# Optimization experiments

Hardware: AMD Instinct MI355X
Metric: run time of the kernel (lower is better)

Reference implementation:

```python
import jax, jax.numpy as jnp
import numpy as np

D_MODEL = 2048
HEADS = 16
HEAD_DIM = D_MODEL // HEADS
INNER = 8192
SEQ = 2048
EPS = 1e-5


def _layernorm(x, g, b):
    mu = jnp.mean(x, axis=-1, keepdims=True)
    var = jnp.mean(jnp.square(x - mu), axis=-1, keepdims=True)
    return (x - mu) * jax.lax.rsqrt(var + EPS) * g + b


def setup_inputs() -> dict:
    key = jax.random.key(0)
    ks = jax.random.split(key, 10)
    s = 0.02
    return {
        "x": jax.random.normal(ks[0], (1, SEQ, D_MODEL), dtype=jnp.float32),
        "C_w": jax.random.normal(ks[1], (D_MODEL, 3 * D_MODEL), dtype=jnp.float32) * s,
        "C_b": jnp.zeros((3 * D_MODEL,), dtype=jnp.float32),
        "lin_w": jax.random.normal(ks[2], (D_MODEL, D_MODEL), dtype=jnp.float32) * s,
        "lin_b": jnp.zeros((D_MODEL,), dtype=jnp.float32),
        "ff1_w": jax.random.normal(ks[3], (D_MODEL, INNER), dtype=jnp.float32) * s,
        "ff1_b": jnp.zeros((INNER,), dtype=jnp.float32),
        "ff2_w": jax.random.normal(ks[4], (INNER, D_MODEL), dtype=jnp.float32) * s,
        "ff2_b": jnp.zeros((D_MODEL,), dtype=jnp.float32),
        "ln1_g": jnp.ones((D_MODEL,), dtype=jnp.float32),
        "ln1_b": jnp.zeros((D_MODEL,), dtype=jnp.float32),
        "ln2_g": jnp.ones((D_MODEL,), dtype=jnp.float32),
        "ln2_b": jnp.zeros((D_MODEL,), dtype=jnp.float32),
    }


def reference(x, C_w, C_b, lin_w, lin_b, ff1_w, ff1_b, ff2_w, ff2_b,
              ln1_g, ln1_b, ln2_g, ln2_b):
    b, s, d = x.shape
    c = x @ C_w + C_b                       # [b, s, 3d]
    q, k, v = jnp.split(c, 3, axis=2)
    q = q.reshape(b, s, HEADS, HEAD_DIM)
    k = k.reshape(b, s, HEADS, HEAD_DIM)
    v = v.reshape(b, s, HEADS, HEAD_DIM)
    # NOTE: source scales by sqrt(d_model), NOT sqrt(head_dim)
    qk = jnp.einsum('bqhd,bkhd->bhqk', q, k) / jnp.sqrt(jnp.float32(d))
    causal = jnp.tril(jnp.ones((s, s), dtype=bool))  # [s, s]
    qk = jnp.where(causal[None, None, :, :], qk, -jnp.inf)
    scores = jax.nn.softmax(qk, axis=3)
    out = jnp.einsum('bhqk,bkhd->bqhd', scores, v).reshape(b, s, d)
    attn = out @ lin_w + lin_b
    h1 = _layernorm(x + attn, ln1_g, ln1_b)
    ff = jax.nn.gelu(h1 @ ff1_w + ff1_b, approximate=False) @ ff2_w + ff2_b
    return _layernorm(h1 + ff, ln2_g, ln2_b)
```

## Files before the change

### kernel.cpp

```cpp
#include <hip/hip_runtime.h>
#include <hip/hip_bf16.h>

#define SEQ 2048
#define DM 2048
#define NH 16
#define HD 128
#define FF 8192

typedef float f4v __attribute__((ext_vector_type(4)));
typedef short s8v __attribute__((ext_vector_type(8)));

__device__ __forceinline__ ushort f2bf(float f) {
  unsigned int x = __float_as_uint(f);
  unsigned int r = (x + 0x7FFFu + ((x >> 16) & 1u)) >> 16;
  return (ushort)r;
}

#define AS1 __attribute__((address_space(1)))
#define AS3 __attribute__((address_space(3)))
__device__ __forceinline__ void load16_lds(const ushort* g, ushort* l) {
  __builtin_amdgcn_global_load_lds((const AS1 unsigned int*)g, (AS3 unsigned int*)l, 16, 0, 0);
}

__global__ __launch_bounds__(256) void k_cvt(const float* __restrict__ in,
                                             ushort* __restrict__ out, int n4) {
  int i = blockIdx.x * 256 + threadIdx.x;
  if (i >= n4) return;
  f4v v = reinterpret_cast<const f4v*>(in)[i];
  ushort4 u;
  u.x = f2bf(v[0]); u.y = f2bf(v[1]); u.z = f2bf(v[2]); u.w = f2bf(v[3]);
  reinterpret_cast<ushort4*>(out)[i] = u;
}

__global__ __launch_bounds__(256) void k_tr(const float* __restrict__ W,
                                            ushort* __restrict__ Wt,
                                            int K, int N) {
  __shared__ float tile[32][36];
  int t = threadIdx.x;
  int n0 = blockIdx.x * 32, k0 = blockIdx.y * 32;
  int lr = t >> 3, lc = (t & 7) * 4;
  *(f4v*)&tile[lr][lc] = *(const f4v*)&W[(size_t)(k0 + lr) * N + n0 + lc];
  __syncthreads();
  int sn = t >> 3, sk = (t & 7) * 4;
  ushort4 u;
  u.x = f2bf(tile[sk + 0][sn]);
  u.y = f2bf(tile[sk + 1][sn]);
  u.z = f2bf(tile[sk + 2][sn]);
  u.w = f2bf(tile[sk + 3][sn]);
  *(ushort4*)&Wt[(size_t)(n0 + sn) * K + k0 + sk] = u;
}

__global__ __launch_bounds__(256) void k_gemm(const ushort* __restrict__ A,
                                              const ushort* __restrict__ Bt,
                                              const float* __restrict__ bias,
                                              float* __restrict__ Cf,
                                              ushort* __restrict__ Cb,
                                              int M, int N, int K, int gelu) {
  __shared__ ushort As[128 * 64];
  __shared__ ushort Bs[128 * 64];
  const int m0 = blockIdx.y * 128, n0 = blockIdx.x * 128;
  const int t = threadIdx.x;
  const int wave = t >> 6, lane = t & 63;
  const int wm = (wave >> 1) * 64, wn = (wave & 1) * 64;
  const int quad = lane >> 4, l16 = lane & 15;
  const int kchunk = K / gridDim.z;
  const int kbeg = blockIdx.z * kchunk, kend = kbeg + kchunk;
  if (Cf && gridDim.z > 1) Cf += (size_t)blockIdx.z * M * N;
  f4v acc[4][4] = {};
  const int srow = lane >> 3;
  const int scg = (lane & 7) ^ srow;
  const ushort* gA = A + (size_t)(m0 + wave * 32 + srow) * K + scg * 8;
  const ushort* gB = Bt + (size_t)(n0 + wave * 32 + srow) * K + scg * 8;
  ushort* lA = &As[(wave * 32) * 64];
  ushort* lB = &Bs[(wave * 32) * 64];

  for (int k0 = kbeg; k0 < kend; k0 += 64) {
#pragma unroll
    for (int p = 0; p < 4; ++p) {
      load16_lds(gA + (size_t)p * 8 * K + k0, lA + p * 8 * 64);
      load16_lds(gB + (size_t)p * 8 * K + k0, lB + p * 8 * 64);
    }
    __syncthreads();
#pragma unroll
    for (int kk = 0; kk < 64; kk += 32) {
      s8v af[4], bf[4];
#pragma unroll
      for (int i = 0; i < 4; ++i) {
        int ar = wm + i * 16 + l16;
        af[i] = *(const s8v*)&As[ar * 64 + ((((kk >> 3) + quad) ^ (ar & 7)) * 8)];
      }
#pragma unroll
      for (int j = 0; j < 4; ++j) {
        int br = wn + j * 16 + l16;
        bf[j] = *(const s8v*)&Bs[br * 64 + ((((kk >> 3) + quad) ^ (br & 7)) * 8)];
      }
#pragma unroll
      for (int i = 0; i < 4; ++i)
#pragma unroll
        for (int j = 0; j < 4; ++j)
          acc[i][j] = __builtin_amdgcn_mfma_f32_16x16x32_bf16(af[i], bf[j], acc[i][j], 0, 0, 0);
    }
    __syncthreads();
  }
#pragma unroll
  for (int i = 0; i < 4; ++i) {
    int rbase = m0 + wm + i * 16 + quad * 4;
#pragma unroll
    for (int j = 0; j < 4; ++j) {
      int cidx = n0 + wn + j * 16 + l16;
      float b = bias ? bias[cidx] : 0.0f;
#pragma unroll
      for (int r = 0; r < 4; ++r) {
        float v = acc[i][j][r] + b;
        if (gelu) v = 0.5f * v * (1.0f + erff(v * 0.70710678118654752f));
        if (Cf) Cf[(size_t)(rbase + r) * N + cidx] = v;
        if (Cb) Cb[(size_t)(rbase + r) * N + cidx] = f2bf(v);
      }
    }
  }
}

__global__ __launch_bounds__(256) void k_attn_mfma(const ushort* __restrict__ qkv,
                                                   ushort* __restrict__ ctx) {
  __shared__ ushort Ks[64][136];
  __shared__ ushort Vt[128][72];
  __shared__ ushort Ps[4][16][72];
  const int idx = blockIdx.x;
  const int h = idx & (NH - 1);
  const int qt = (SEQ / 64 - 1) - (idx >> 4);
  const int q0 = qt * 64;
  const int t = threadIdx.x;
  const int wave = t >> 6, lane = t & 63;
  const int quad = lane >> 4, l16 = lane & 15;
  const float scale = 0.022097086912079608f;

  s8v aq[4];
  {
    const ushort* qp = qkv + (size_t)(q0 + 16 * wave + l16) * (3 * DM) + h * HD + quad * 8;
#pragma unroll
    for (int ks = 0; ks < 4; ++ks)
      aq[ks] = *(const s8v*)(qp + ks * 32);
  }
  f4v acc_o[8] = {};
  float m_r[4], l_r[4];
#pragma unroll
  for (int r = 0; r < 4; ++r) { m_r[r] = -1e30f; l_r[r] = 0.0f; }

  for (int kt = 0; kt <= qt; ++kt) {
    const int k0 = kt * 64;
    __syncthreads();
    {
      const ushort* kp = qkv + (size_t)k0 * (3 * DM) + DM + h * HD;
#pragma unroll
      for (int i = 0; i < 4; ++i) {
        int ch = t + i * 256;
        int row = ch >> 4, c8 = (ch & 15) * 8;
        *(s8v*)&Ks[row][c8] = *(const s8v*)(kp + (size_t)row * (3 * DM) + c8);
      }
      const ushort* vp = qkv + (size_t)k0 * (3 * DM) + 2 * DM + h * HD;
#pragma unroll
      for (int i = 0; i < 4; ++i) {
        int id = t + i * 256;
        int d = id & 127, sg = id >> 7;
        ushort e0 = vp[(size_t)(sg * 8 + 0) * (3 * DM) + d];
        ushort e1 = vp[(size_t)(sg * 8 + 1) * (3 * DM) + d];
        ushort e2 = vp[(size_t)(sg * 8 + 2) * (3 * DM) + d];
        ushort e3 = vp[(size_t)(sg * 8 + 3) * (3 * DM) + d];
        ushort e4 = vp[(size_t)(sg * 8 + 4) * (3 * DM) + d];
        ushort e5 = vp[(size_t)(sg * 8 + 5) * (3 * DM) + d];
        ushort e6 = vp[(size_t)(sg * 8 + 6) * (3 * DM) + d];
        ushort e7 = vp[(size_t)(sg * 8 + 7) * (3 * DM) + d];
        uint4 pk;
        pk.x = (uint)e0 | ((uint)e1 << 16);
        pk.y = (uint)e2 | ((uint)e3 << 16);
        pk.z = (uint)e4 | ((uint)e5 << 16);
        pk.w = (uint)e6 | ((uint)e7 << 16);
        *(uint4*)&Vt[d][sg * 8] = pk;
      }
    }
    __syncthreads();

    f4v sacc[4] = {};
#pragma unroll
    for (int ks = 0; ks < 4; ++ks) {
      s8v bk[4];
#pragma unroll
      for (int j = 0; j < 4; ++j)
        bk[j] = *(const s8v*)&Ks[j * 16 + l16][ks * 32 + quad * 8];
#pragma unroll
      for (int j = 0; j < 4; ++j)
        sacc[j] = __builtin_amdgcn_mfma_f32_16x16x32_bf16(aq[ks], bk[j], sacc[j], 0, 0, 0);
    }
    if (kt == qt) {
#pragma unroll
      for (int j = 0; j < 4; ++j)
#pragma unroll
        for (int r = 0; r < 4; ++r) {
          int lrow = 16 * wave + quad * 4 + r;
          int lcol = j * 16 + l16;
          sacc[j][r] = (lcol > lrow) ? -1e30f : sacc[j][r] * scale;
        }
    } else {
#pragma unroll
      for (int j = 0; j < 4; ++j)
#pragma unroll
        for (int r = 0; r < 4; ++r) sacc[j][r] *= scale;
    }
    float alpha[4];
#pragma unroll
    for (int r = 0; r < 4; ++r) {
      float mx = fmaxf(fmaxf(sacc[0][r], sacc[1][r]), fmaxf(sacc[2][r], sacc[3][r]));
      mx = fmaxf(mx, __shfl_xor(mx, 1));
      mx = fmaxf(mx, __shfl_xor(mx, 2));
      mx = fmaxf(mx, __shfl_xor(mx, 4));
      mx = fmaxf(mx, __shfl_xor(mx, 8));
      float mn = fmaxf(m_r[r], mx);
      alpha[r] = __expf(m_r[r] - mn);
      m_r[r] = mn;
      float ps = 0.0f;
#pragma unroll
      for (int j = 0; j < 4; ++j) {
        float p = __expf(sacc[j][r] - mn);
        sacc[j][r] = p;
        ps += p;
      }
      ps += __shfl_xor(ps, 1);
      ps += __shfl_xor(ps, 2);
      ps += __shfl_xor(ps, 4);
      ps += __shfl_xor(ps, 8);
      l_r[r] = l_r[r] * alpha[r] + ps;
    }
#pragma unroll
    for (int j = 0; j < 4; ++j)
#pragma unroll
      for (int r = 0; r < 4; ++r)
        Ps[wave][quad * 4 + r][j * 16 + l16] = f2bf(sacc[j][r]);
#pragma unroll
    for (int nd = 0; nd < 8; ++nd)
#pragma unroll
      for (int r = 0; r < 4; ++r) acc_o[nd][r] *= alpha[r];
#pragma unroll
    for (int ks2 = 0; ks2 < 2; ++ks2) {
      s8v ap = *(const s8v*)&Ps[wave][l16][ks2 * 32 + quad * 8];
#pragma unroll
      for (int nd = 0; nd < 8; ++nd) {
        s8v bv = *(const s8v*)&Vt[nd * 16 + l16][ks2 * 32 + quad * 8];
        acc_o[nd] = __builtin_amdgcn_mfma_f32_16x16x32_bf16(ap, bv, acc_o[nd], 0, 0, 0);
      }
    }
  }
  float rl[4];
#pragma unroll
  for (int r = 0; r < 4; ++r) rl[r] = 1.0f / l_r[r];
#pragma unroll
  for (int nd = 0; nd < 8; ++nd) {
    int col = h * HD + nd * 16 + l16;
#pragma unroll
    for (int r = 0; r < 4; ++r) {
      int row = q0 + 16 * wave + quad * 4 + r;
      ctx[(size_t)row * DM + col] = f2bf(acc_o[nd][r] * rl[r]);
    }
  }
}

__global__ __launch_bounds__(256) void k_ln_sk(const float* __restrict__ A,
                                               const float* __restrict__ P, int np,
                                               const float* __restrict__ bias,
                                               const float* __restrict__ g,
                                               const float* __restrict__ be,
                                               float* __restrict__ outf,
                                               ushort* __restrict__ outb) {
  int row = blockIdx.x;
  int t = threadIdx.x;
  const f4v* av = reinterpret_cast<const f4v*>(A + (size_t)row * DM);
  f4v x0 = av[t];
  f4v x1 = av[t + 256];
  for (int s = 0; s < np; ++s) {
    const f4v* pv = reinterpret_cast<const f4v*>(P + (size_t)s * SEQ * DM + (size_t)row * DM);
    x0 += pv[t];
    x1 += pv[t + 256];
  }
  const f4v* bb = reinterpret_cast<const f4v*>(bias);
  x0 += bb[t];
  x1 += bb[t + 256];
  float s = x0[0] + x0[1] + x0[2] + x0[3] + x1[0] + x1[1] + x1[2] + x1[3];
  float q = x0[0]*x0[0] + x0[1]*x0[1] + x0[2]*x0[2] + x0[3]*x0[3]
          + x1[0]*x1[0] + x1[1]*x1[1] + x1[2]*x1[2] + x1[3]*x1[3];
#pragma unroll
  for (int off = 32; off; off >>= 1) {
    s += __shfl_down(s, off, 64);
    q += __shfl_down(q, off, 64);
  }
  __shared__ float rs[4], rq[4];
  if ((t & 63) == 0) { rs[t >> 6] = s; rq[t >> 6] = q; }
  __syncthreads();
  s = rs[0] + rs[1] + rs[2] + rs[3];
  q = rq[0] + rq[1] + rq[2] + rq[3];
  float mu = s * (1.0f / DM);
  float var = q * (1.0f / DM) - mu * mu;
  float rstd = rsqrtf(var + 1e-5f);
  const f4v* gv = reinterpret_cast<const f4v*>(g);
  const f4v* bev = reinterpret_cast<const f4v*>(be);
  f4v y0 = (x0 - mu) * rstd * gv[t] + bev[t];
  f4v y1 = (x1 - mu) * rstd * gv[t + 256] + bev[t + 256];
  reinterpret_cast<f4v*>(outf + (size_t)row * DM)[t] = y0;
  reinterpret_cast<f4v*>(outf + (size_t)row * DM)[t + 256] = y1;
  if (outb) {
    ushort4 u0, u1;
    u0.x = f2bf(y0[0]); u0.y = f2bf(y0[1]); u0.z = f2bf(y0[2]); u0.w = f2bf(y0[3]);
    u1.x = f2bf(y1[0]); u1.y = f2bf(y1[1]); u1.z = f2bf(y1[2]); u1.w = f2bf(y1[3]);
    reinterpret_cast<ushort4*>(outb + (size_t)row * DM)[t] = u0;
    reinterpret_cast<ushort4*>(outb + (size_t)row * DM)[t + 256] = u1;
  }
}

extern "C" void kernel_launch(void* const* d_in, const int* in_sizes, int n_in,
                              void* d_out, int out_size, void* d_ws, size_t ws_size,
                              hipStream_t stream) {
  const float* x     = (const float*)d_in[0];
  const float* C_w   = (const float*)d_in[1];
  const float* C_b   = (const float*)d_in[2];
  const float* lin_w = (const float*)d_in[3];
  const float* lin_b = (const float*)d_in[4];
  const float* ff1_w = (const float*)d_in[5];
  const float* ff1_b = (const float*)d_in[6];
  const float* ff2_w = (const float*)d_in[7];
  const float* ff2_b = (const float*)d_in[8];
  const float* ln1g  = (const float*)d_in[9];
  const float* ln1b  = (const float*)d_in[10];
  const float* ln2g  = (const float*)d_in[11];
  const float* ln2b  = (const float*)d_in[12];

  char* ws = (char*)d_ws;
  size_t off = 0;
  auto take = [&](size_t bytes) {
    char* p = ws + off;
    off += (bytes + 255) & ~(size_t)255;
    return p;
  };
  ushort* Wt   = (ushort*)take((size_t)FF * DM * 2);
  ushort* qkvb = (ushort*)take((size_t)SEQ * 3 * DM * 2);
  ushort* xb   = (ushort*)take((size_t)SEQ * DM * 2);
  ushort* ctxb = (ushort*)take((size_t)SEQ * DM * 2);
  ushort* bigb = (ushort*)take((size_t)SEQ * FF * 2);
  float*  h1   = (float*) take((size_t)SEQ * DM * 4);
  float*  part = (float*) take((size_t)4 * SEQ * DM * 4);

  k_cvt<<<SEQ * DM / 1024, 256, 0, stream>>>(x, xb, SEQ * DM / 4);
  k_tr<<<dim3(3 * DM / 32, DM / 32), 256, 0, stream>>>(C_w, Wt, DM, 3 * DM);
  k_gemm<<<dim3(3 * DM / 128, SEQ / 128, 1), 256, 0, stream>>>(xb, Wt, C_b, nullptr, qkvb, SEQ, 3 * DM, DM, 0);
  k_attn_mfma<<<dim3((SEQ / 64) * NH), 256, 0, stream>>>(qkvb, ctxb);
  k_tr<<<dim3(DM / 32, DM / 32), 256, 0, stream>>>(lin_w, Wt, DM, DM);
  k_gemm<<<dim3(DM / 128, SEQ / 128, 4), 256, 0, stream>>>(ctxb, Wt, nullptr, part, nullptr, SEQ, DM, DM, 0);
  k_ln_sk<<<SEQ, 256, 0, stream>>>(x, part, 4, lin_b, ln1g, ln1b, h1, xb);
  k_tr<<<dim3(FF / 32, DM / 32), 256, 0, stream>>>(ff1_w, Wt, DM, FF);
  k_gemm<<<dim3(FF / 128, SEQ / 128, 1), 256, 0, stream>>>(xb, Wt, ff1_b, nullptr, bigb, SEQ, FF, DM, 1);
  k_tr<<<dim3(DM / 32, FF / 32), 256, 0, stream>>>(ff2_w, Wt, FF, DM);
  k_gemm<<<dim3(DM / 128, SEQ / 128, 4), 256, 0, stream>>>(bigb, Wt, nullptr, part, nullptr, SEQ, DM, FF, 0);
  k_ln_sk<<<SEQ, 256, 0, stream>>>(h1, part, 4, ff2_b, ln2g, ln2b, (float*)d_out, (ushort*)nullptr);
}
```

Baseline: 636.8 us.

## Replace GEMM with 256x256 tile, 4-stage LDS pipeline and split B loads

Replaces the 128x128 single-buffered GEMM with a 256x256-tile, 512-thread kernel. It uses a 4-deep ring of 32-wide K tiles loaded asynchronously via global_load_lds, waits on vmcnt counters, and raises wave priority around MFMA blocks. The larger tile raises arithmetic intensity per LDS byte, and the prefetch pipeline overlaps global loads with compute. The costs are more registers (8x4 accumulators), fewer blocks per grid (e.g. 8x8x4 = 256 for the split-K GEMMs), and delicate hand-written waitcnt/barrier logic.

Result: faster. 609.1 us (-4.3%).

```diff
diff --git a/kernel.cpp b/kernel.cpp
--- a/kernel.cpp
+++ b/kernel.cpp
@@ -50,60 +50,96 @@
   *(ushort4*)&Wt[(size_t)(n0 + sn) * K + k0 + sk] = u;
 }
 
-__global__ __launch_bounds__(256) void k_gemm(const ushort* __restrict__ A,
-                                              const ushort* __restrict__ Bt,
-                                              const float* __restrict__ bias,
-                                              float* __restrict__ Cf,
-                                              ushort* __restrict__ Cb,
-                                              int M, int N, int K, int gelu) {
-  __shared__ ushort As[128 * 64];
-  __shared__ ushort Bs[128 * 64];
-  const int m0 = blockIdx.y * 128, n0 = blockIdx.x * 128;
+#define GBM 256
+#define GBN 256
+#define GBK 32
+#define TILE_SH (GBM * GBK)
+
+__global__ __launch_bounds__(512, 2) void k_gemm256(
+    const ushort* __restrict__ A, const ushort* __restrict__ Bt,
+    const float* __restrict__ bias, float* __restrict__ Cf,
+    ushort* __restrict__ Cb, int M, int N, int K, int gelu) {
+  __shared__ ushort As[4 * TILE_SH];
+  __shared__ ushort Bs[4 * TILE_SH];
+  const int m0 = blockIdx.y * GBM, n0 = blockIdx.x * GBN;
   const int t = threadIdx.x;
-  const int wave = t >> 6, lane = t & 63;
-  const int wm = (wave >> 1) * 64, wn = (wave & 1) * 64;
+  const int w = t >> 6, lane = t & 63;
   const int quad = lane >> 4, l16 = lane & 15;
+  const int wm = (w >> 2) * 128, wn = (w & 3) * 64;
   const int kchunk = K / gridDim.z;
-  const int kbeg = blockIdx.z * kchunk, kend = kbeg + kchunk;
+  const int kbeg = blockIdx.z * kchunk;
+  const int NT = kchunk / GBK;
   if (Cf && gridDim.z > 1) Cf += (size_t)blockIdx.z * M * N;
-  f4v acc[4][4] = {};
-  const int srow = lane >> 3;
-  const int scg = (lane & 7) ^ srow;
-  const ushort* gA = A + (size_t)(m0 + wave * 32 + srow) * K + scg * 8;
-  const ushort* gB = Bt + (size_t)(n0 + wave * 32 + srow) * K + scg * 8;
-  ushort* lA = &As[(wave * 32) * 64];
-  ushort* lB = &Bs[(wave * 32) * 64];
-
-  for (int k0 = kbeg; k0 < kend; k0 += 64) {
-#pragma unroll
-    for (int p = 0; p < 4; ++p) {
-      load16_lds(gA + (size_t)p * 8 * K + k0, lA + p * 8 * 64);
-      load16_lds(gB + (size_t)p * 8 * K + k0, lB + p * 8 * 64);
-    }
-    __syncthreads();
-#pragma unroll
-    for (int kk = 0; kk < 64; kk += 32) {
-      s8v af[4], bf[4];
-#pragma unroll
-      for (int i = 0; i < 4; ++i) {
-        int ar = wm + i * 16 + l16;
-        af[i] = *(const s8v*)&As[ar * 64 + ((((kk >> 3) + quad) ^ (ar & 7)) * 8)];
-      }
-#pragma unroll
-      for (int j = 0; j < 4; ++j) {
-        int br = wn + j * 16 + l16;
-        bf[j] = *(const s8v*)&Bs[br * 64 + ((((kk >> 3) + quad) ^ (br & 7)) * 8)];
-      }
-#pragma unroll
-      for (int i = 0; i < 4; ++i)
-#pragma unroll
-        for (int j = 0; j < 4; ++j)
-          acc[i][j] = __builtin_amdgcn_mfma_f32_16x16x32_bf16(af[i], bf[j], acc[i][j], 0, 0, 0);
-    }
-    __syncthreads();
-  }
-#pragma unroll
-  for (int i = 0; i < 4; ++i) {
+
+  const int srow = lane >> 2;
+  const int cg = (lane & 3) ^ ((srow >> 1) & 3);
+  const ushort* gA = A + (size_t)(m0 + w * 32 + srow) * K + kbeg + cg * 8;
+  const ushort* gB = Bt + (size_t)(n0 + w * 32 + srow) * K + kbeg + cg * 8;
+  const int swz = (quad ^ ((l16 >> 1) & 3)) * 8;
+  const int baseA = (wm + l16) * GBK + swz;
+  const int baseB = (wn + l16) * GBK + swz;
+
+  f4v acc[8][4] = {};
+
+#pragma unroll
+  for (int pt = 0; pt < 3; ++pt) {
+    ushort* lA = &As[pt * TILE_SH + (w * 32) * GBK];
+    ushort* lB = &Bs[pt * TILE_SH + (w * 32) * GBK];
+    load16_lds(gA + pt * GBK, lA);
+    load16_lds(gA + pt * GBK + (size_t)16 * K, lA + 16 * GBK);
+    load16_lds(gB + pt * GBK, lB);
+    load16_lds(gB + pt * GBK + (size_t)16 * K, lB + 16 * GBK);
+  }
+  asm volatile("s_waitcnt vmcnt(8)\n\ts_barrier" ::: "memory");
+
+  for (int tt = 0; tt < NT; ++tt) {
+    const ushort* At = &As[(tt & 3) * TILE_SH];
+    const ushort* Bc = &Bs[(tt & 3) * TILE_SH];
+    const int nb = (tt + 3) & 3;
+    s8v a[8], b0, b1;
+#pragma unroll
+    for (int i = 0; i < 8; ++i)
+      a[i] = *(const s8v*)&At[baseA + i * 16 * GBK];
+    b0 = *(const s8v*)&Bc[baseB + 0 * 16 * GBK];
+    b1 = *(const s8v*)&Bc[baseB + 1 * 16 * GBK];
+    if (tt + 3 < NT) {
+      ushort* lA = &As[nb * TILE_SH + (w * 32) * GBK];
+      load16_lds(gA + (size_t)(tt + 3) * GBK, lA);
+      load16_lds(gA + (size_t)(tt + 3) * GBK + (size_t)16 * K, lA + 16 * GBK);
+    }
+    __builtin_amdgcn_s_setprio(1);
+#pragma unroll
+    for (int i = 0; i < 8; ++i) {
+      acc[i][0] = __builtin_amdgcn_mfma_f32_16x16x32_bf16(a[i], b0, acc[i][0], 0, 0, 0);
+      acc[i][1] = __builtin_amdgcn_mfma_f32_16x16x32_bf16(a[i], b1, acc[i][1], 0, 0, 0);
+    }
+    __builtin_amdgcn_s_setprio(0);
+    asm volatile("s_barrier" ::: "memory");
+    s8v b2 = *(const s8v*)&Bc[baseB + 2 * 16 * GBK];
+    s8v b3 = *(const s8v*)&Bc[baseB + 3 * 16 * GBK];
+    if (tt + 3 < NT) {
+      ushort* lB = &Bs[nb * TILE_SH + (w * 32) * GBK];
+      load16_lds(gB + (size_t)(tt + 3) * GBK, lB);
+      load16_lds(gB + (size_t)(tt + 3) * GBK + (size_t)16 * K, lB + 16 * GBK);
+    }
+    __builtin_amdgcn_s_setprio(1);
+#pragma unroll
+    for (int i = 0; i < 8; ++i) {
+      acc[i][2] = __builtin_amdgcn_mfma_f32_16x16x32_bf16(a[i], b2, acc[i][2], 0, 0, 0);
+      acc[i][3] = __builtin_amdgcn_mfma_f32_16x16x32_bf16(a[i], b3, acc[i][3], 0, 0, 0);
+    }
+    __builtin_amdgcn_s_setprio(0);
+    if (tt + 4 <= NT) {
+      asm volatile("s_waitcnt vmcnt(8)\n\ts_barrier" ::: "memory");
+    } else if (tt + 3 <= NT) {
+      asm volatile("s_waitcnt vmcnt(4)\n\ts_barrier" ::: "memory");
+    } else if (tt + 2 <= NT) {
+      asm volatile("s_waitcnt vmcnt(0)\n\ts_barrier" ::: "memory");
+    }
+  }
+
+#pragma unroll
+  for (int i = 0; i < 8; ++i) {
     int rbase = m0 + wm + i * 16 + quad * 4;
 #pragma unroll
     for (int j = 0; j < 4; ++j) {
@@ -348,14 +384,14 @@
 
   k_cvt<<<SEQ * DM / 1024, 256, 0, stream>>>(x, xb, SEQ * DM / 4);
   k_tr<<<dim3(3 * DM / 32, DM / 32), 256, 0, stream>>>(C_w, Wt, DM, 3 * DM);
-  k_gemm<<<dim3(3 * DM / 128, SEQ / 128, 1), 256, 0, stream>>>(xb, Wt, C_b, nullptr, qkvb, SEQ, 3 * DM, DM, 0);
+  k_gemm256<<<dim3(3 * DM / 256, SEQ / 256, 1), 512, 0, stream>>>(xb, Wt, C_b, nullptr, qkvb, SEQ, 3 * DM, DM, 0);
   k_attn_mfma<<<dim3((SEQ / 64) * NH), 256, 0, stream>>>(qkvb, ctxb);
   k_tr<<<dim3(DM / 32, DM / 32), 256, 0, stream>>>(lin_w, Wt, DM, DM);
-  k_gemm<<<dim3(DM / 128, SEQ / 128, 4), 256, 0, stream>>>(ctxb, Wt, nullptr, part, nullptr, SEQ, DM, DM, 0);
+  k_gemm256<<<dim3(DM / 256, SEQ / 256, 4), 512, 0, stream>>>(ctxb, Wt, nullptr, part, nullptr, SEQ, DM, DM, 0);
   k_ln_sk<<<SEQ, 256, 0, stream>>>(x, part, 4, lin_b, ln1g, ln1b, h1, xb);
   k_tr<<<dim3(FF / 32, DM / 32), 256, 0, stream>>>(ff1_w, Wt, DM, FF);
-  k_gemm<<<dim3(FF / 128, SEQ / 128, 1), 256, 0, stream>>>(xb, Wt, ff1_b, nullptr, bigb, SEQ, FF, DM, 1);
+  k_gemm256<<<dim3(FF / 256, SEQ / 256, 1), 512, 0, stream>>>(xb, Wt, ff1_b, nullptr, bigb, SEQ, FF, DM, 1);
   k_tr<<<dim3(DM / 32, FF / 32), 256, 0, stream>>>(ff2_w, Wt, FF, DM);
-  k_gemm<<<dim3(DM / 128, SEQ / 128, 4), 256, 0, stream>>>(bigb, Wt, nullptr, part, nullptr, SEQ, DM, FF, 0);
+  k_gemm256<<<dim3(DM / 256, SEQ / 256, 4), 512, 0, stream>>>(bigb, Wt, nullptr, part, nullptr, SEQ, DM, FF, 0);
   k_ln_sk<<<SEQ, 256, 0, stream>>>(h1, part, 4, ff2_b, ln2g, ln2b, (float*)d_out, (ushort*)nullptr);
 }
```
